# Kernel tuning notes

Measured on AMD Instinct MI355X. Metric: run time of the kernel, lower is better.

Reference implementation:

```python
import jax, jax.numpy as jnp
import numpy as np

ERR_OK = 0.1  # tolerance constant ('err_ok' is an undefined free var in the original source)

N = 20_000_000
F = 5

def setup_inputs() -> dict:
    key = jax.random.key(0)
    k1, k2 = jax.random.split(key)
    inputs = jax.random.normal(k1, (N, F), dtype=jnp.float32)
    targets = jax.random.normal(k2, (N, 1), dtype=jnp.float32)
    return {"inputs": inputs, "targets": targets}

def reference(inputs, targets):
    # per-row: abs(inputs[:,0]-inputs[:,4]) if |inputs[:,4]-inputs[:,2]| < err_ok
    #          else abs(inputs[:,0]-targets[:,0]); then mean over rows.
    cond = jnp.abs(inputs[:, 4] - inputs[:, 2]) < ERR_OK
    diff = jnp.where(cond, inputs[:, 0] - inputs[:, 4], inputs[:, 0] - targets[:, 0])
    return jnp.mean(jnp.abs(diff))
```

## Files before the change

kernel.cpp:

```cpp
#include <hip/hip_runtime.h>


#define NBLOCKS 2048
#define NTHREADS 256

__device__ __forceinline__ float row_term(float c0, float c2, float c4, float tgt) {
    float d = (fabsf(c4 - c2) < 0.1f) ? (c0 - c4) : (c0 - tgt);
    return fabsf(d);
}

__global__ __launch_bounds__(NTHREADS) void loss_partial(
    const float* __restrict__ in, const float* __restrict__ tg,
    float* __restrict__ partial, long long nrows)
{
    const long long ngroups = nrows >> 2;
    const long long tid = (long long)blockIdx.x * blockDim.x + threadIdx.x;
    const long long stride = (long long)gridDim.x * blockDim.x;
    const float4* __restrict__ in4 = (const float4*)in;
    const float4* __restrict__ tg4 = (const float4*)tg;

    float sum = 0.0f;
    for (long long g = tid; g < ngroups; g += stride) {
        const float4 v0 = in4[5 * g + 0];
        const float4 v1 = in4[5 * g + 1];
        const float4 v2 = in4[5 * g + 2];
        const float4 v3 = in4[5 * g + 3];
        const float4 v4 = in4[5 * g + 4];
        const float4 t  = tg4[g];

        sum += row_term(v0.x, v0.z, v1.x, t.x);
        sum += row_term(v1.y, v1.w, v2.y, t.y);
        sum += row_term(v2.z, v3.x, v3.z, t.z);
        sum += row_term(v3.w, v4.y, v4.w, t.w);
    }

    for (long long r = (ngroups << 2) + tid; r < nrows; r += stride) {
        sum += row_term(in[5 * r + 0], in[5 * r + 2], in[5 * r + 4], tg[r]);
    }

    #pragma unroll
    for (int off = 32; off > 0; off >>= 1)
        sum += __shfl_down(sum, off, 64);

    __shared__ float wsum[NTHREADS / 64];
    const int lane = threadIdx.x & 63;
    const int wave = threadIdx.x >> 6;
    if (lane == 0) wsum[wave] = sum;
    __syncthreads();
    if (threadIdx.x == 0) {
        float s = 0.0f;
        #pragma unroll
        for (int w = 0; w < NTHREADS / 64; ++w) s += wsum[w];
        partial[blockIdx.x] = s;
    }
}

__global__ __launch_bounds__(NTHREADS) void loss_final(
    const float* __restrict__ partial, int nparts,
    float* __restrict__ out, long long nrows)
{
    float sum = 0.0f;
    for (int i = threadIdx.x; i < nparts; i += NTHREADS) sum += partial[i];

    #pragma unroll
    for (int off = 32; off > 0; off >>= 1)
        sum += __shfl_down(sum, off, 64);

    __shared__ float wsum[NTHREADS / 64];
    const int lane = threadIdx.x & 63;
    const int wave = threadIdx.x >> 6;
    if (lane == 0) wsum[wave] = sum;
    __syncthreads();
    if (threadIdx.x == 0) {
        float s = 0.0f;
        #pragma unroll
        for (int w = 0; w < NTHREADS / 64; ++w) s += wsum[w];
        out[0] = s / (float)nrows;
    }
}

extern "C" void kernel_launch(void* const* d_in, const int* in_sizes, int n_in,
                              void* d_out, int out_size, void* d_ws, size_t ws_size,
                              hipStream_t stream) {
    const float* inputs  = (const float*)d_in[0];
    const float* targets = (const float*)d_in[1];
    float* out = (float*)d_out;
    float* partial = (float*)d_ws;

    const long long nrows = (long long)in_sizes[0] / 5;

    loss_partial<<<NBLOCKS, NTHREADS, 0, stream>>>(inputs, targets, partial, nrows);
    loss_final<<<1, NTHREADS, 0, stream>>>(partial, NBLOCKS, out, nrows);
}
```

Baseline: 556.3 us.

## Stage input rows through shared memory tiles for coalesced loads

```diff
diff --git a/kernel.cpp b/kernel.cpp
--- a/kernel.cpp
+++ b/kernel.cpp
@@ -3,6 +3,8 @@
 
 #define NBLOCKS 2048
 #define NTHREADS 256
+#define ROWS_PER_TILE 1024
+#define F4_PER_TILE 1280
 
 __device__ __forceinline__ float row_term(float c0, float c2, float c4, float tgt) {
     float d = (fabsf(c4 - c2) < 0.1f) ? (c0 - c4) : (c0 - tgt);
@@ -13,29 +15,42 @@
     const float* __restrict__ in, const float* __restrict__ tg,
     float* __restrict__ partial, long long nrows)
 {
-    const long long ngroups = nrows >> 2;
-    const long long tid = (long long)blockIdx.x * blockDim.x + threadIdx.x;
-    const long long stride = (long long)gridDim.x * blockDim.x;
+    __shared__ float4 tile4[F4_PER_TILE];
+    float* tile = (float*)tile4;
+
     const float4* __restrict__ in4 = (const float4*)in;
-    const float4* __restrict__ tg4 = (const float4*)tg;
+    const int tid = threadIdx.x;
 
     float sum = 0.0f;
-    for (long long g = tid; g < ngroups; g += stride) {
-        const float4 v0 = in4[5 * g + 0];
-        const float4 v1 = in4[5 * g + 1];
-        const float4 v2 = in4[5 * g + 2];
-        const float4 v3 = in4[5 * g + 3];
-        const float4 v4 = in4[5 * g + 4];
-        const float4 t  = tg4[g];
 
-        sum += row_term(v0.x, v0.z, v1.x, t.x);
-        sum += row_term(v1.y, v1.w, v2.y, t.y);
-        sum += row_term(v2.z, v3.x, v3.z, t.z);
-        sum += row_term(v3.w, v4.y, v4.w, t.w);
+    const long long ntiles = nrows / ROWS_PER_TILE;
+    for (long long t = blockIdx.x; t < ntiles; t += gridDim.x) {
+        const float4* __restrict__ src = in4 + t * F4_PER_TILE;
+        #pragma unroll
+        for (int k = 0; k < 5; ++k)
+            tile4[k * NTHREADS + tid] = src[k * NTHREADS + tid];
+        __syncthreads();
+
+        const long long rowbase = t * ROWS_PER_TILE;
+        const float* __restrict__ tgb = tg + rowbase;
+        #pragma unroll
+        for (int j = 0; j < 4; ++j) {
+            const int r = tid + j * NTHREADS;
+            const float c0 = tile[5 * r + 0];
+            const float c2 = tile[5 * r + 2];
+            const float c4 = tile[5 * r + 4];
+            const float tv = tgb[r];
+            sum += row_term(c0, c2, c4, tv);
+        }
+        __syncthreads();
     }
 
-    for (long long r = (ngroups << 2) + tid; r < nrows; r += stride) {
-        sum += row_term(in[5 * r + 0], in[5 * r + 2], in[5 * r + 4], tg[r]);
+    {
+        const long long start = ntiles * ROWS_PER_TILE;
+        const long long gtid = (long long)blockIdx.x * NTHREADS + tid;
+        const long long gstride = (long long)gridDim.x * NTHREADS;
+        for (long long r = start + gtid; r < nrows; r += gstride)
+            sum += row_term(in[5 * r + 0], in[5 * r + 2], in[5 * r + 4], tg[r]);
     }
 
     #pragma unroll
@@ -43,11 +58,11 @@
         sum += __shfl_down(sum, off, 64);
 
     __shared__ float wsum[NTHREADS / 64];
-    const int lane = threadIdx.x & 63;
-    const int wave = threadIdx.x >> 6;
+    const int lane = tid & 63;
+    const int wave = tid >> 6;
     if (lane == 0) wsum[wave] = sum;
     __syncthreads();
-    if (threadIdx.x == 0) {
+    if (tid == 0) {
         float s = 0.0f;
         #pragma unroll
         for (int w = 0; w < NTHREADS / 64; ++w) s += wsum[w];
```

Measured after the change: 558.5 us. Within noise of the previous version (+0.4%).
